# Performance work log

Hardware: AMD Instinct MI355X
Metric: run time of the kernel (lower is better)

## Reference

```python
import jax, jax.numpy as jnp
import numpy as np

ALPHA = 3.0
NITERS = 15
POWER_ITERS = 20
ROOTS = [np.cos(np.pi * (2 * i + 1) / (2 * NITERS)) for i in range(NITERS)]


def batch_conv2d(inputs, kernels):
    # inputs: [B,1,H,W], kernels: [B,1,3,3]; per-sample 3x3 stencil via grouped conv
    B, _, H, W = inputs.shape
    out = jax.lax.conv_general_dilated(
        inputs.reshape(1, B, H, W), kernels,
        window_strides=(1, 1), padding=((1, 1), (1, 1)),
        feature_group_count=B,
        dimension_numbers=("NCHW", "OIHW", "NCHW"))
    return out.reshape(B, 1, H, W)


def setup_inputs() -> dict:
    key = jax.random.key(0)
    k1, k2, k3, k4 = jax.random.split(key, 4)
    B, H, W = 64, 512, 512
    x = jax.random.normal(k1, (B, 1, H, W), dtype=jnp.float32)
    f = jax.random.normal(k2, (B, 1, H, W), dtype=jnp.float32)
    kernelA = jax.random.normal(k3, (B, 1, 3, 3), dtype=jnp.float32)
    u = jax.random.normal(k4, (B, 1, H, W), dtype=jnp.float32)
    return {"x": x, "f": f, "kernelA": kernelA, "u": u}


def reference(x, f, kernelA, u):
    # Power iteration to estimate the dominant eigenvalue magnitude m per sample
    for _ in range(POWER_ITERS):
        y = batch_conv2d(u, kernelA)
        m = jnp.max(jnp.abs(y), axis=(2, 3), keepdims=True)  # [B,1,1,1]
        u = y / m
    # Chebyshev step sizes over the band [m/alpha, m]
    taus = jnp.stack(
        [2.0 / (m + m / ALPHA - (m / ALPHA - m) * r) for r in ROOTS])  # [niters,B,1,1,1]

    def cheby_step(xc, tau):
        Ax = batch_conv2d(xc, kernelA)
        return xc + tau * (f - Ax), None

    x, _ = jax.lax.scan(cheby_step, x, taus)
    return x
```

## Files before the change

kernel.cpp:

```cpp
#include <hip/hip_runtime.h>

#define BB 64
#define HH 512
#define WW 512
#define PLANE (HH * WW)
#define R 32
#define NSTRIPE (HH / R)
#define N_CHEBY 15
#define FD 5
#define STEPS (R + 3 * FD - 1)
#define LOADCUT (R + 2 * FD - 1)

struct Sl { float a, b, c, d; };

__device__ __forceinline__ void racc(const Sl& s, float k0, float k1, float k2,
                                     float& o0, float& o1) {
    o0 = fmaf(k0, s.a, fmaf(k1, s.b, fmaf(k2, s.c, o0)));
    o1 = fmaf(k0, s.b, fmaf(k1, s.c, fmaf(k2, s.d, o1)));
}

__device__ __forceinline__ Sl ldsl(const float* pl, int row, int c2, bool ok) {
    Sl s = {0.f, 0.f, 0.f, 0.f};
    if (ok) {
        const float* rp = pl + (size_t)row * WW;
        float2 v = *reinterpret_cast<const float2*>(rp + c2);
        s.b = v.x; s.c = v.y;
        if (c2 > 0)      s.a = rp[c2 - 1];
        if (c2 + 2 < WW) s.d = rp[c2 + 2];
    }
    return s;
}

__device__ __forceinline__ void softbar() {
    __asm__ volatile("s_waitcnt lgkmcnt(0)" ::: "memory");
    __builtin_amdgcn_s_barrier();
}

__global__ __launch_bounds__(256, 4) void conv_fused5(
    const float* __restrict__ in, const float* __restrict__ kern,
    const float* __restrict__ pm_prev, float* __restrict__ out,
    float* __restrict__ pmw, float* __restrict__ pmz)
{
    const int b = blockIdx.y, stripe = blockIdx.x, ytop = stripe * R;
    const int t = threadIdx.x, c2 = t << 1;

    __shared__ float re[FD - 1][2][258], ro[FD - 1][2][258];
    __shared__ float sred[8];
    __shared__ float sinv;

    if (t < 2 * (FD - 1)) {
        const int l = t >> 1, par = t & 1;
        re[l][par][0] = 0.f; re[l][par][257] = 0.f;
        ro[l][par][0] = 0.f; ro[l][par][257] = 0.f;
    }
    if (pm_prev && t < 64) {
        float v = (t < NSTRIPE) ? pm_prev[b * NSTRIPE + t] : 0.f;
#pragma unroll
        for (int o = 8; o; o >>= 1) v = fmaxf(v, __shfl_xor(v, o, 64));
        if (t == 0) sinv = 1.f / v;
    }
    __syncthreads();
    const float invv = pm_prev ? sinv : 1.f;

    const float* kb = kern + b * 9;
    const float k00=kb[0],k01=kb[1],k02=kb[2],k10=kb[3],k11=kb[4],k12=kb[5],
                k20=kb[6],k21=kb[7],k22=kb[8];
    const float* ip = in + (size_t)b * PLANE;
    float* op = out ? out + (size_t)b * PLANE : nullptr;

    Sl u2 = {0,0,0,0}, u1 = {0,0,0,0};
    Sl ltp[FD - 1], lmd[FD - 1];
    float own0[FD - 1], own1[FD - 1];
#pragma unroll
    for (int l = 0; l < FD - 1; ++l) {
        ltp[l] = Sl{0,0,0,0}; lmd[l] = Sl{0,0,0,0};
        own0[l] = 0.f; own1[l] = 0.f;
    }
    float mz = 0.f, mw = 0.f;
    Sl u0 = ldsl(ip, ytop - FD, c2, (unsigned)(ytop - FD) < HH);

#pragma unroll 2
    for (int p = 0; p < STEPS; ++p) {
        const int yu = ytop - FD + p;
        Sl un = ldsl(ip, yu + 1, c2, ((unsigned)(yu + 1) < HH) && (p < LOADCUT));

        const int rpar = (p + 1) & 1, wpar = p & 1;
        Sl am[FD - 1];
#pragma unroll
        for (int l = 0; l < FD - 1; ++l) {
            am[l].a = ro[l][rpar][t];
            am[l].b = own0[l];
            am[l].c = own1[l];
            am[l].d = re[l][rpar][2 + t];
        }

        float v0[FD], v1[FD];
        {
            float s0 = 0.f, s1 = 0.f;
            racc(u2, k00,k01,k02, s0,s1);
            racc(u1, k10,k11,k12, s0,s1);
            racc(u0, k20,k21,k22, s0,s1);
            const int y = yu - 1;
            const bool act = (y >= ytop - (FD-1)) && (y <= ytop + R + FD - 2)
                          && ((unsigned)y < HH);
            v0[0] = act ? s0 * invv : 0.f;
            v1[0] = act ? s1 * invv : 0.f;
        }
#pragma unroll
        for (int j = 2; j <= FD; ++j) {
            float s0 = 0.f, s1 = 0.f;
            racc(ltp[j-2], k00,k01,k02, s0,s1);
            racc(lmd[j-2], k10,k11,k12, s0,s1);
            racc(am[j-2],  k20,k21,k22, s0,s1);
            const int y = yu - (2*j - 1);
            if (j < FD) {
                const bool act = (y >= ytop - (FD-j)) && (y <= ytop + R + FD - j - 1)
                              && ((unsigned)y < HH);
                v0[j-1] = act ? s0 : 0.f;
                v1[j-1] = act ? s1 : 0.f;
                if (j == FD - 1)
                    mz = fmaxf(mz, fmaxf(fabsf(v0[j-1]), fabsf(v1[j-1])));
            } else {
                if (y >= ytop && y < ytop + R) {
                    mw = fmaxf(mw, fmaxf(fabsf(s0), fabsf(s1)));
                    if (op)
                        *reinterpret_cast<float2*>(op + (size_t)y * WW + c2) =
                            make_float2(s0, s1);
                }
            }
        }
#pragma unroll
        for (int l = 0; l < FD - 1; ++l) {
            re[l][wpar][1 + t] = v0[l];
            ro[l][wpar][1 + t] = v1[l];
            ltp[l] = lmd[l]; lmd[l] = am[l];
            own0[l] = v0[l]; own1[l] = v1[l];
        }
        u2 = u1; u1 = u0; u0 = un;
        softbar();
    }

#pragma unroll
    for (int o = 32; o; o >>= 1) {
        mz = fmaxf(mz, __shfl_xor(mz, o, 64));
        mw = fmaxf(mw, __shfl_xor(mw, o, 64));
    }
    if ((t & 63) == 0) { sred[t >> 6] = mz; sred[4 + (t >> 6)] = mw; }
    __syncthreads();
    if (t == 0) {
        pmz[b * NSTRIPE + stripe] =
            fmaxf(fmaxf(sred[0], sred[1]), fmaxf(sred[2], sred[3]));
        pmw[b * NSTRIPE + stripe] =
            fmaxf(fmaxf(sred[4], sred[5]), fmaxf(sred[6], sred[7]));
    }
}

__global__ __launch_bounds__(64) void tau_fused(
    const float* __restrict__ pmz, const float* __restrict__ pmw,
    float* __restrict__ taus)
{
    const int b = blockIdx.x, t = threadIdx.x;
    float vz = (t < NSTRIPE) ? pmz[b * NSTRIPE + t] : 0.f;
    float vw = (t < NSTRIPE) ? pmw[b * NSTRIPE + t] : 0.f;
#pragma unroll
    for (int o = 8; o; o >>= 1) {
        vz = fmaxf(vz, __shfl_xor(vz, o, 64));
        vw = fmaxf(vw, __shfl_xor(vw, o, 64));
    }
    if (t < N_CHEBY) {
        const float m = vw / vz;
        const double rr = cos(M_PI * (2.0 * t + 1.0) / (2.0 * N_CHEBY));
        const float denom = m + m / 3.0f - (m / 3.0f - m) * (float)rr;
        taus[t * BB + b] = 2.0f / denom;
    }
}

__global__ __launch_bounds__(256, 4) void cheby_fused5(
    const float* __restrict__ xin, const float* __restrict__ fin,
    const float* __restrict__ kern, const float* __restrict__ tau5,
    float* __restrict__ xout)
{
    const int b = blockIdx.y, stripe = blockIdx.x, ytop = stripe * R;
    const int t = threadIdx.x, c2 = t << 1;

    __shared__ float re[FD - 1][2][258], ro[FD - 1][2][258];

    if (t < 2 * (FD - 1)) {
        const int l = t >> 1, par = t & 1;
        re[l][par][0] = 0.f; re[l][par][257] = 0.f;
        ro[l][par][0] = 0.f; ro[l][par][257] = 0.f;
    }
    __syncthreads();

    const float* kb = kern + b * 9;
    const float k00=kb[0],k01=kb[1],k02=kb[2],k10=kb[3],k11=kb[4],k12=kb[5],
                k20=kb[6],k21=kb[7],k22=kb[8];
    float tau[FD];
#pragma unroll
    for (int j = 0; j < FD; ++j) tau[j] = tau5[j * BB + b];

    const float* xp = xin + (size_t)b * PLANE;
    const float* fp = fin + (size_t)b * PLANE;
    float* op = xout + (size_t)b * PLANE;

    Sl u2 = {0,0,0,0}, u1 = {0,0,0,0};
    Sl ltp[FD - 1], lmd[FD - 1];
    float own0[FD - 1], own1[FD - 1];
#pragma unroll
    for (int l = 0; l < FD - 1; ++l) {
        ltp[l] = Sl{0,0,0,0}; lmd[l] = Sl{0,0,0,0};
        own0[l] = 0.f; own1[l] = 0.f;
    }
    float2 fh[2 * FD - 1];
#pragma unroll
    for (int k = 1; k < 2 * FD - 1; ++k) fh[k] = make_float2(0.f, 0.f);

    Sl u0 = ldsl(xp, ytop - FD, c2, (unsigned)(ytop - FD) < HH);
    {
        const int yf = ytop - FD - 1;
        fh[0] = ((unsigned)yf < HH)
            ? *reinterpret_cast<const float2*>(fp + (size_t)yf * WW + c2)
            : make_float2(0.f, 0.f);
    }

#pragma unroll 2
    for (int p = 0; p < STEPS; ++p) {
        const int yu = ytop - FD + p;
        const bool ldok = (p < LOADCUT);
        Sl un = ldsl(xp, yu + 1, c2, ((unsigned)(yu + 1) < HH) && ldok);
        const float2 fn = (((unsigned)yu < HH) && ldok)
            ? *reinterpret_cast<const float2*>(fp + (size_t)yu * WW + c2)
            : make_float2(0.f, 0.f);

        const int rpar = (p + 1) & 1, wpar = p & 1;
        Sl am[FD - 1];
#pragma unroll
        for (int l = 0; l < FD - 1; ++l) {
            am[l].a = ro[l][rpar][t];
            am[l].b = own0[l];
            am[l].c = own1[l];
            am[l].d = re[l][rpar][2 + t];
        }

        float v0[FD], v1[FD];
        {
            float s0 = 0.f, s1 = 0.f;
            racc(u2, k00,k01,k02, s0,s1);
            racc(u1, k10,k11,k12, s0,s1);
            racc(u0, k20,k21,k22, s0,s1);
            const int y = yu - 1;
            const bool act = (y >= ytop - (FD-1)) && (y <= ytop + R + FD - 2)
                          && ((unsigned)y < HH);
            v0[0] = act ? fmaf(tau[0], fh[0].x - s0, u1.b) : 0.f;
            v1[0] = act ? fmaf(tau[0], fh[0].y - s1, u1.c) : 0.f;
        }
#pragma unroll
        for (int j = 2; j <= FD; ++j) {
            float s0 = 0.f, s1 = 0.f;
            racc(ltp[j-2], k00,k01,k02, s0,s1);
            racc(lmd[j-2], k10,k11,k12, s0,s1);
            racc(am[j-2],  k20,k21,k22, s0,s1);
            const int y = yu - (2*j - 1);
            const float2 fv = fh[2*(j-1)];
            if (j < FD) {
                const bool act = (y >= ytop - (FD-j)) && (y <= ytop + R + FD - j - 1)
                              && ((unsigned)y < HH);
                v0[j-1] = act ? fmaf(tau[j-1], fv.x - s0, lmd[j-2].b) : 0.f;
                v1[j-1] = act ? fmaf(tau[j-1], fv.y - s1, lmd[j-2].c) : 0.f;
            } else {
                if (y >= ytop && y < ytop + R) {
                    const float o0 = fmaf(tau[FD-1], fv.x - s0, lmd[j-2].b);
                    const float o1 = fmaf(tau[FD-1], fv.y - s1, lmd[j-2].c);
                    *reinterpret_cast<float2*>(op + (size_t)y * WW + c2) =
                        make_float2(o0, o1);
                }
            }
        }
#pragma unroll
        for (int l = 0; l < FD - 1; ++l) {
            re[l][wpar][1 + t] = v0[l];
            ro[l][wpar][1 + t] = v1[l];
            ltp[l] = lmd[l]; lmd[l] = am[l];
            own0[l] = v0[l]; own1[l] = v1[l];
        }
        u2 = u1; u1 = u0; u0 = un;
#pragma unroll
        for (int k = 2 * FD - 2; k > 0; --k) fh[k] = fh[k - 1];
        fh[0] = fn;
        softbar();
    }
}

extern "C" void kernel_launch(void* const* d_in, const int* in_sizes, int n_in,
                              void* d_out, int out_size, void* d_ws, size_t ws_size,
                              hipStream_t stream)
{
    const float* x_in = (const float*)d_in[0];
    const float* f_in = (const float*)d_in[1];
    const float* k_in = (const float*)d_in[2];
    const float* u_in = (const float*)d_in[3];
    float* out = (float*)d_out;

    float* bufA = (float*)d_ws;
    float* pmW0 = bufA + (size_t)BB * PLANE;
    float* pmW1 = pmW0 + BB * NSTRIPE;
    float* pmZ  = pmW1 + BB * NSTRIPE;
    float* taus = pmZ  + BB * NSTRIPE;

    dim3 blk(256), grd(NSTRIPE, BB);

    const float* src = u_in;
    for (int g = 0; g < 4; ++g) {
        float* dst = (g == 3) ? nullptr : ((g & 1) ? out : bufA);
        const float* pprev = g ? ((g & 1) ? pmW0 : pmW1) : nullptr;
        float* pw = (g & 1) ? pmW1 : pmW0;
        conv_fused5<<<grd, blk, 0, stream>>>(src, k_in, pprev, dst, pw, pmZ);
        if (dst) src = dst;
    }

    tau_fused<<<BB, 64, 0, stream>>>(pmZ, pmW1, taus);

    cheby_fused5<<<grd, blk, 0, stream>>>(x_in, f_in, k_in, taus + 0 * BB, out);
    cheby_fused5<<<grd, blk, 0, stream>>>(out,  f_in, k_in, taus + 5 * BB, bufA);
    cheby_fused5<<<grd, blk, 0, stream>>>(bufA, f_in, k_in, taus + 10 * BB, out);
}
```

Baseline: 367.4 us.

## Deepen temporal fusion: 10-step power passes, 8+7 Chebyshev passes, taller stripes

Templates the fused stencil kernels on the fusion depth. Power iteration now runs as two 10-deep passes instead of four 5-deep ones, and the Chebyshev steps run as 8+7 instead of 5+5+5. Stripe height doubles to 64 rows so the growing halo overhead stays bounded. This cuts full-plane global reads and writes and kernel launches, at the cost of more registers and LDS per block, lower occupancy (launch bounds lowered to 2), and more redundant halo compute.

Result: slower. 391.4 us (+6.5%).

```diff
diff --git a/kernel.cpp b/kernel.cpp
--- a/kernel.cpp
+++ b/kernel.cpp
@@ -4,12 +4,9 @@
 #define HH 512
 #define WW 512
 #define PLANE (HH * WW)
-#define R 32
+#define R 64
 #define NSTRIPE (HH / R)
 #define N_CHEBY 15
-#define FD 5
-#define STEPS (R + 3 * FD - 1)
-#define LOADCUT (R + 2 * FD - 1)
 
 struct Sl { float a, b, c, d; };
 
@@ -36,7 +33,8 @@
     __builtin_amdgcn_s_barrier();
 }
 
-__global__ __launch_bounds__(256, 4) void conv_fused5(
+template<int FDv>
+__global__ __launch_bounds__(256, 2) void conv_fusedN(
     const float* __restrict__ in, const float* __restrict__ kern,
     const float* __restrict__ pm_prev, float* __restrict__ out,
     float* __restrict__ pmw, float* __restrict__ pmz)
@@ -44,11 +42,11 @@
     const int b = blockIdx.y, stripe = blockIdx.x, ytop = stripe * R;
     const int t = threadIdx.x, c2 = t << 1;
 
-    __shared__ float re[FD - 1][2][258], ro[FD - 1][2][258];
+    __shared__ float re[FDv - 1][2][258], ro[FDv - 1][2][258];
     __shared__ float sred[8];
     __shared__ float sinv;
 
-    if (t < 2 * (FD - 1)) {
+    if (t < 2 * (FDv - 1)) {
         const int l = t >> 1, par = t & 1;
         re[l][par][0] = 0.f; re[l][par][257] = 0.f;
         ro[l][par][0] = 0.f; ro[l][par][257] = 0.f;
@@ -69,56 +67,58 @@
     float* op = out ? out + (size_t)b * PLANE : nullptr;
 
     Sl u2 = {0,0,0,0}, u1 = {0,0,0,0};
-    Sl ltp[FD - 1], lmd[FD - 1];
-    float own0[FD - 1], own1[FD - 1];
-#pragma unroll
-    for (int l = 0; l < FD - 1; ++l) {
+    Sl ltp[FDv - 1], lmd[FDv - 1];
+    float own0[FDv - 1], own1[FDv - 1];
+#pragma unroll
+    for (int l = 0; l < FDv - 1; ++l) {
         ltp[l] = Sl{0,0,0,0}; lmd[l] = Sl{0,0,0,0};
         own0[l] = 0.f; own1[l] = 0.f;
     }
     float mz = 0.f, mw = 0.f;
-    Sl u0 = ldsl(ip, ytop - FD, c2, (unsigned)(ytop - FD) < HH);
-
+    Sl u0 = ldsl(ip, ytop - FDv, c2, (unsigned)(ytop - FDv) < HH);
+
+    const int STEPS   = R + 3 * FDv - 1;
+    const int LOADCUT = R + 2 * FDv - 1;
 #pragma unroll 2
     for (int p = 0; p < STEPS; ++p) {
-        const int yu = ytop - FD + p;
+        const int yu = ytop - FDv + p;
         Sl un = ldsl(ip, yu + 1, c2, ((unsigned)(yu + 1) < HH) && (p < LOADCUT));
 
         const int rpar = (p + 1) & 1, wpar = p & 1;
-        Sl am[FD - 1];
-#pragma unroll
-        for (int l = 0; l < FD - 1; ++l) {
+        Sl am[FDv - 1];
+#pragma unroll
+        for (int l = 0; l < FDv - 1; ++l) {
             am[l].a = ro[l][rpar][t];
             am[l].b = own0[l];
             am[l].c = own1[l];
             am[l].d = re[l][rpar][2 + t];
         }
 
-        float v0[FD], v1[FD];
+        float v0[FDv], v1[FDv];
         {
             float s0 = 0.f, s1 = 0.f;
             racc(u2, k00,k01,k02, s0,s1);
             racc(u1, k10,k11,k12, s0,s1);
             racc(u0, k20,k21,k22, s0,s1);
             const int y = yu - 1;
-            const bool act = (y >= ytop - (FD-1)) && (y <= ytop + R + FD - 2)
+            const bool act = (y >= ytop - (FDv-1)) && (y <= ytop + R + FDv - 2)
                           && ((unsigned)y < HH);
             v0[0] = act ? s0 * invv : 0.f;
             v1[0] = act ? s1 * invv : 0.f;
         }
 #pragma unroll
-        for (int j = 2; j <= FD; ++j) {
+        for (int j = 2; j <= FDv; ++j) {
             float s0 = 0.f, s1 = 0.f;
             racc(ltp[j-2], k00,k01,k02, s0,s1);
             racc(lmd[j-2], k10,k11,k12, s0,s1);
             racc(am[j-2],  k20,k21,k22, s0,s1);
             const int y = yu - (2*j - 1);
-            if (j < FD) {
-                const bool act = (y >= ytop - (FD-j)) && (y <= ytop + R + FD - j - 1)
+            if (j < FDv) {
+                const bool act = (y >= ytop - (FDv-j)) && (y <= ytop + R + FDv - j - 1)
                               && ((unsigned)y < HH);
                 v0[j-1] = act ? s0 : 0.f;
                 v1[j-1] = act ? s1 : 0.f;
-                if (j == FD - 1)
+                if (j == FDv - 1)
                     mz = fmaxf(mz, fmaxf(fabsf(v0[j-1]), fabsf(v1[j-1])));
             } else {
                 if (y >= ytop && y < ytop + R) {
@@ -130,7 +130,7 @@
             }
         }
 #pragma unroll
-        for (int l = 0; l < FD - 1; ++l) {
+        for (int l = 0; l < FDv - 1; ++l) {
             re[l][wpar][1 + t] = v0[l];
             ro[l][wpar][1 + t] = v1[l];
             ltp[l] = lmd[l]; lmd[l] = am[l];
@@ -175,17 +175,18 @@
     }
 }
 
-__global__ __launch_bounds__(256, 4) void cheby_fused5(
+template<int FDv>
+__global__ __launch_bounds__(256, 2) void cheby_fusedN(
     const float* __restrict__ xin, const float* __restrict__ fin,
-    const float* __restrict__ kern, const float* __restrict__ tau5,
+    const float* __restrict__ kern, const float* __restrict__ tauv,
     float* __restrict__ xout)
 {
     const int b = blockIdx.y, stripe = blockIdx.x, ytop = stripe * R;
     const int t = threadIdx.x, c2 = t << 1;
 
-    __shared__ float re[FD - 1][2][258], ro[FD - 1][2][258];
-
-    if (t < 2 * (FD - 1)) {
+    __shared__ float re[FDv - 1][2][258], ro[FDv - 1][2][258];
+
+    if (t < 2 * (FDv - 1)) {
         const int l = t >> 1, par = t & 1;
         re[l][par][0] = 0.f; re[l][par][257] = 0.f;
         ro[l][par][0] = 0.f; ro[l][par][257] = 0.f;
@@ -195,37 +196,39 @@
     const float* kb = kern + b * 9;
     const float k00=kb[0],k01=kb[1],k02=kb[2],k10=kb[3],k11=kb[4],k12=kb[5],
                 k20=kb[6],k21=kb[7],k22=kb[8];
-    float tau[FD];
-#pragma unroll
-    for (int j = 0; j < FD; ++j) tau[j] = tau5[j * BB + b];
+    float tau[FDv];
+#pragma unroll
+    for (int j = 0; j < FDv; ++j) tau[j] = tauv[j * BB + b];
 
     const float* xp = xin + (size_t)b * PLANE;
     const float* fp = fin + (size_t)b * PLANE;
     float* op = xout + (size_t)b * PLANE;
 
     Sl u2 = {0,0,0,0}, u1 = {0,0,0,0};
-    Sl ltp[FD - 1], lmd[FD - 1];
-    float own0[FD - 1], own1[FD - 1];
-#pragma unroll
-    for (int l = 0; l < FD - 1; ++l) {
+    Sl ltp[FDv - 1], lmd[FDv - 1];
+    float own0[FDv - 1], own1[FDv - 1];
+#pragma unroll
+    for (int l = 0; l < FDv - 1; ++l) {
         ltp[l] = Sl{0,0,0,0}; lmd[l] = Sl{0,0,0,0};
         own0[l] = 0.f; own1[l] = 0.f;
     }
-    float2 fh[2 * FD - 1];
-#pragma unroll
-    for (int k = 1; k < 2 * FD - 1; ++k) fh[k] = make_float2(0.f, 0.f);
-
-    Sl u0 = ldsl(xp, ytop - FD, c2, (unsigned)(ytop - FD) < HH);
+    float2 fh[2 * FDv - 1];
+#pragma unroll
+    for (int k = 1; k < 2 * FDv - 1; ++k) fh[k] = make_float2(0.f, 0.f);
+
+    Sl u0 = ldsl(xp, ytop - FDv, c2, (unsigned)(ytop - FDv) < HH);
     {
-        const int yf = ytop - FD - 1;
+        const int yf = ytop - FDv - 1;
         fh[0] = ((unsigned)yf < HH)
             ? *reinterpret_cast<const float2*>(fp + (size_t)yf * WW + c2)
             : make_float2(0.f, 0.f);
     }
 
+    const int STEPS   = R + 3 * FDv - 1;
+    const int LOADCUT = R + 2 * FDv - 1;
 #pragma unroll 2
     for (int p = 0; p < STEPS; ++p) {
-        const int yu = ytop - FD + p;
+        const int yu = ytop - FDv + p;
         const bool ldok = (p < LOADCUT);
         Sl un = ldsl(xp, yu + 1, c2, ((unsigned)(yu + 1) < HH) && ldok);
         const float2 fn = (((unsigned)yu < HH) && ldok)
@@ -233,51 +236,51 @@
             : make_float2(0.f, 0.f);
 
         const int rpar = (p + 1) & 1, wpar = p & 1;
-        Sl am[FD - 1];
-#pragma unroll
-        for (int l = 0; l < FD - 1; ++l) {
+        Sl am[FDv - 1];
+#pragma unroll
+        for (int l = 0; l < FDv - 1; ++l) {
             am[l].a = ro[l][rpar][t];
             am[l].b = own0[l];
             am[l].c = own1[l];
             am[l].d = re[l][rpar][2 + t];
         }
 
-        float v0[FD], v1[FD];
+        float v0[FDv], v1[FDv];
         {
             float s0 = 0.f, s1 = 0.f;
             racc(u2, k00,k01,k02, s0,s1);
             racc(u1, k10,k11,k12, s0,s1);
             racc(u0, k20,k21,k22, s0,s1);
             const int y = yu - 1;
-            const bool act = (y >= ytop - (FD-1)) && (y <= ytop + R + FD - 2)
+            const bool act = (y >= ytop - (FDv-1)) && (y <= ytop + R + FDv - 2)
                           && ((unsigned)y < HH);
             v0[0] = act ? fmaf(tau[0], fh[0].x - s0, u1.b) : 0.f;
             v1[0] = act ? fmaf(tau[0], fh[0].y - s1, u1.c) : 0.f;
         }
 #pragma unroll
-        for (int j = 2; j <= FD; ++j) {
+        for (int j = 2; j <= FDv; ++j) {
             float s0 = 0.f, s1 = 0.f;
             racc(ltp[j-2], k00,k01,k02, s0,s1);
             racc(lmd[j-2], k10,k11,k12, s0,s1);
             racc(am[j-2],  k20,k21,k22, s0,s1);
             const int y = yu - (2*j - 1);
             const float2 fv = fh[2*(j-1)];
-            if (j < FD) {
-                const bool act = (y >= ytop - (FD-j)) && (y <= ytop + R + FD - j - 1)
+            if (j < FDv) {
+                const bool act = (y >= ytop - (FDv-j)) && (y <= ytop + R + FDv - j - 1)
                               && ((unsigned)y < HH);
                 v0[j-1] = act ? fmaf(tau[j-1], fv.x - s0, lmd[j-2].b) : 0.f;
                 v1[j-1] = act ? fmaf(tau[j-1], fv.y - s1, lmd[j-2].c) : 0.f;
             } else {
                 if (y >= ytop && y < ytop + R) {
-                    const float o0 = fmaf(tau[FD-1], fv.x - s0, lmd[j-2].b);
-                    const float o1 = fmaf(tau[FD-1], fv.y - s1, lmd[j-2].c);
+                    const float o0 = fmaf(tau[FDv-1], fv.x - s0, lmd[j-2].b);
+                    const float o1 = fmaf(tau[FDv-1], fv.y - s1, lmd[j-2].c);
                     *reinterpret_cast<float2*>(op + (size_t)y * WW + c2) =
                         make_float2(o0, o1);
                 }
             }
         }
 #pragma unroll
-        for (int l = 0; l < FD - 1; ++l) {
+        for (int l = 0; l < FDv - 1; ++l) {
             re[l][wpar][1 + t] = v0[l];
             ro[l][wpar][1 + t] = v1[l];
             ltp[l] = lmd[l]; lmd[l] = am[l];
@@ -285,7 +288,7 @@
         }
         u2 = u1; u1 = u0; u0 = un;
 #pragma unroll
-        for (int k = 2 * FD - 2; k > 0; --k) fh[k] = fh[k - 1];
+        for (int k = 2 * FDv - 2; k > 0; --k) fh[k] = fh[k - 1];
         fh[0] = fn;
         softbar();
     }
@@ -309,18 +312,11 @@
 
     dim3 blk(256), grd(NSTRIPE, BB);
 
-    const float* src = u_in;
-    for (int g = 0; g < 4; ++g) {
-        float* dst = (g == 3) ? nullptr : ((g & 1) ? out : bufA);
-        const float* pprev = g ? ((g & 1) ? pmW0 : pmW1) : nullptr;
-        float* pw = (g & 1) ? pmW1 : pmW0;
-        conv_fused5<<<grd, blk, 0, stream>>>(src, k_in, pprev, dst, pw, pmZ);
-        if (dst) src = dst;
-    }
+    conv_fusedN<10><<<grd, blk, 0, stream>>>(u_in, k_in, nullptr, bufA, pmW0, pmZ);
+    conv_fusedN<10><<<grd, blk, 0, stream>>>(bufA, k_in, pmW0, nullptr, pmW1, pmZ);
 
     tau_fused<<<BB, 64, 0, stream>>>(pmZ, pmW1, taus);
 
-    cheby_fused5<<<grd, blk, 0, stream>>>(x_in, f_in, k_in, taus + 0 * BB, out);
-    cheby_fused5<<<grd, blk, 0, stream>>>(out,  f_in, k_in, taus + 5 * BB, bufA);
-    cheby_fused5<<<grd, blk, 0, stream>>>(bufA, f_in, k_in, taus + 10 * BB, out);
-}
+    cheby_fusedN<8><<<grd, blk, 0, stream>>>(x_in, f_in, k_in, taus, bufA);
+    cheby_fusedN<7><<<grd, blk, 0, stream>>>(bufA, f_in, k_in, taus + 8 * BB, out);
+}
```
